# Kernel optimization log

Measured on AMD Instinct MI355X. Metric: run time of the kernel, lower is better.

## Reference

```python
import jax, jax.numpy as jnp
import numpy as np

RADIUS = 1.0
NSAMPLE = 32


def setup_inputs() -> dict:
    key = jax.random.key(0)
    k1, k2, k3, k4, k5 = jax.random.split(key, 5)
    B, Nb, M, K, C = 2, 2048, 64, 216, 32
    N = B * Nb
    # points in a 20m cube
    xyz = jax.random.uniform(k1, (N, 3), dtype=jnp.float32) * 20.0
    xyz_batch_cnt = jnp.array([Nb, Nb], dtype=jnp.int32)
    # rois: [x,y,z,dx,dy,dz,ry]
    ctr = jax.random.uniform(k2, (B, M, 3), dtype=jnp.float32) * 20.0
    dims = 1.0 + jax.random.uniform(k3, (B, M, 3), dtype=jnp.float32) * 2.0
    ry = jax.random.uniform(k4, (B, M, 1), dtype=jnp.float32) * 6.28
    rois = jnp.concatenate([ctr, dims, ry], axis=-1)
    # 6x6x6 grid points jittered around each roi center
    off = (jax.random.uniform(k5, (B, M, K, 3), dtype=jnp.float32) - 0.5) * 3.0
    new_xyz = ctr[:, :, None, :] + off
    features = jax.random.normal(jax.random.fold_in(key, 7), (N, C), dtype=jnp.float32)
    return {"xyz": xyz, "xyz_batch_cnt": xyz_batch_cnt, "new_xyz": new_xyz,
            "rois": rois, "features": features}


def _query_and_group(xyz, new_xyz, rois, features, B, Nb):
    """Ball query -> ragged compaction (padded to L=N*nsample) -> gather."""
    M, K = new_xyz.shape[1], new_xyz.shape[2]
    MK = M * K
    N = B * Nb
    L = N * NSAMPLE
    xyz_b = xyz.reshape(B, Nb, 3)
    grid = new_xyz.reshape(B, MK, 3)
    # squared distances point -> grid center, (B, Nb, MK)
    d2 = jnp.sum((xyz_b[:, :, None, :] - grid[:, None, :, :]) ** 2, axis=-1)
    # roi bounding sphere: center rois[:,:,:3], radius ||dims||_2 (the `ball` tensor)
    ctr = rois[:, :, :3]
    r2 = jnp.sum(rois[:, :, 3:6] ** 2, axis=-1)          # (B, M)
    d2b = jnp.sum((xyz_b[:, :, None, :] - ctr[:, None, :, :]) ** 2, axis=-1)  # (B,Nb,M)
    in_ball = (d2b <= r2[:, None, :])[:, :, :, None]      # (B,Nb,M,1)
    mask = (d2 <= RADIUS * RADIUS) & jnp.broadcast_to(in_ball, (B, Nb, M, K)).reshape(B, Nb, MK)
    # first-NSAMPLE-in-order selection per point (matches kernel iteration order)
    rank = jnp.cumsum(mask.astype(jnp.int32), axis=2) - 1
    cols = jnp.where(mask & (rank < NSAMPLE), rank, NSAMPLE)  # NSAMPLE = OOB -> dropped
    rows = jnp.broadcast_to(
        jnp.arange(B, dtype=jnp.int32)[:, None, None] * Nb
        + jnp.arange(Nb, dtype=jnp.int32)[None, :, None], (B, Nb, MK))
    flat_idx = jnp.broadcast_to(
        jnp.arange(B, dtype=jnp.int32)[:, None, None] * MK
        + jnp.arange(MK, dtype=jnp.int32)[None, None, :], (B, Nb, MK))
    ball_idx = jnp.full((N, NSAMPLE), -1, dtype=jnp.int32)
    ball_idx = ball_idx.at[rows.reshape(-1), cols.reshape(-1)].set(
        flat_idx.reshape(-1), mode="drop")
    # BallIndice: cumsum compaction of valid (point_idx, grid_idx) pairs, row-major
    valid = (ball_idx > -1).reshape(-1)                  # (L,)
    pos = jnp.cumsum(valid.astype(jnp.int32)) - 1
    pos_w = jnp.where(valid, pos, L)                     # invalid -> OOB -> dropped
    row_ids = jnp.broadcast_to(
        jnp.arange(N, dtype=jnp.int32)[:, None], (N, NSAMPLE)).reshape(-1)
    set_indices = jnp.zeros((L,), jnp.int32).at[pos_w].set(row_ids, mode="drop")
    set_new_indices = jnp.zeros((L,), jnp.int32).at[pos_w].set(
        ball_idx.reshape(-1), mode="drop")
    nind = jnp.sum(valid.astype(jnp.int32))
    vm = (jnp.arange(L) < nind)[:, None].astype(features.dtype)  # padding mask
    # GatherFeature (padded slots zeroed, matching new_zeros semantics)
    group_xyz = xyz[set_indices] * vm
    group_new_xyz = new_xyz.reshape(-1, 3)[set_new_indices] * vm
    group_feat = features[set_indices] * vm
    group_features = jnp.concatenate([group_xyz - group_new_xyz, group_feat], axis=1)
    return group_features, set_new_indices


def reference(xyz, xyz_batch_cnt, new_xyz, rois, features):
    B = xyz_batch_cnt.shape[0]
    Nb = xyz.shape[0] // B
    return _query_and_group(xyz, new_xyz, rois, features, B, Nb)
```

## Files before the change

kernel.cpp:

```cpp
#include <hip/hip_runtime.h>


#pragma clang fp contract(off)

typedef unsigned long long u64;

#define MAXN 4096

__global__ __launch_bounds__(256) void count_kernel(
    const float* __restrict__ xyz, const float* __restrict__ new_xyz,
    const float* __restrict__ rois, int* __restrict__ counts,
    int* __restrict__ ballidx, float* __restrict__ out_all,
    int N, int Nb, int M, int K, int nsample, int totalOut)
{
    __shared__ int plist[4][64];
    const int wave = threadIdx.x >> 6;
    const int lane = threadIdx.x & 63;
    const int r = blockIdx.x * 4 + wave;
    const u64 laneLt = (1ull << lane) - 1ull;

    {
        const int gtid = blockIdx.x * 256 + threadIdx.x;
        const int gthreads = gridDim.x * 256;
        for (int i = gtid; i < totalOut; i += gthreads) out_all[i] = 0.0f;
    }

    if (r >= N) return;

    const int b  = r / Nb;
    const float px = xyz[3 * r + 0];
    const float py = xyz[3 * r + 1];
    const float pz = xyz[3 * r + 2];

    bool pass = false;
    if (lane < M) {
        const float* rp = rois + (size_t)(b * M + lane) * 7;
        const float dx = rp[3], dy = rp[4], dz = rp[5];
        const float r2 = (dx * dx + dy * dy) + dz * dz;
        const float ex = px - rp[0], ey = py - rp[1], ez = pz - rp[2];
        pass = ((ex * ex + ey * ey) + ez * ez) <= r2;
    }
    const u64 roiMask = __ballot(pass);
    if (!roiMask) { if (lane == 0) counts[r] = 0; return; }
    if (pass) plist[wave][__popcll(roiMask & laneLt)] = lane;

    const int P = __popcll(roiMask);
    const int total = P * K;
    const float* nb_ = new_xyz + (size_t)(b * M * K) * 3;
    int* bi = ballidx + (size_t)r * nsample;

    int cnt = 0;
    for (int base = 0; base < total && cnt < nsample; base += 256) {
        bool match[4];
        int jj[4];
        #pragma unroll
        for (int u = 0; u < 4; u++) {
            const int p = base + u * 64 + lane;
            match[u] = false; jj[u] = 0;
            if (p < total) {
                const int ri = p / K;
                const int k  = p - ri * K;
                const int j  = plist[wave][ri] * K + k;
                jj[u] = j;
                const float* gp = nb_ + (size_t)j * 3;
                const float ax = px - gp[0], ay = py - gp[1], az = pz - gp[2];
                match[u] = ((ax * ax + ay * ay) + az * az) <= 1.0f;
            }
        }
        #pragma unroll
        for (int u = 0; u < 4; u++) {
            const u64 mm = __ballot(match[u]);
            const int slot = cnt + __popcll(mm & laneLt);
            if (match[u] && slot < nsample) bi[slot] = jj[u];
            cnt += __popcll(mm);
        }
    }
    if (lane == 0) counts[r] = cnt > nsample ? nsample : cnt;
}

__global__ __launch_bounds__(1024) void scan_kernel(
    const int* __restrict__ counts, int* __restrict__ offsets, int N)
{
    __shared__ int waveAux[16];
    const int t = threadIdx.x;
    const int lane = t & 63;
    const int wid = t >> 6;
    const int base = t * 4;
    int c[4];
    int s = 0;
    #pragma unroll
    for (int i = 0; i < 4; i++) {
        c[i] = (base + i < N) ? counts[base + i] : 0;
        s += c[i];
    }
    int incl = s;
    #pragma unroll
    for (int d = 1; d < 64; d <<= 1) {
        int v = __shfl_up(incl, d, 64);
        if (lane >= d) incl += v;
    }
    if (lane == 63) waveAux[wid] = incl;
    __syncthreads();
    if (t < 16) {
        int v = waveAux[t];
        #pragma unroll
        for (int d = 1; d < 16; d <<= 1) {
            int u = __shfl_up(v, d, 64);
            if (t >= d) v += u;
        }
        waveAux[t] = v;
    }
    __syncthreads();
    int run = (wid ? waveAux[wid - 1] : 0) + incl - s;
    #pragma unroll
    for (int i = 0; i < 4; i++) {
        if (base + i < N) offsets[base + i] = run;
        run += c[i];
    }
}

__global__ __launch_bounds__(256) void emit_kernel(
    const float* __restrict__ xyz, const float* __restrict__ new_xyz,
    const float* __restrict__ features,
    const int* __restrict__ counts, const int* __restrict__ offsets,
    const int* __restrict__ ballidx,
    float* __restrict__ out_feat, float* __restrict__ out_idx,
    int N, int Nb, int M, int K, int C, int nsample)
{
    const int wave = threadIdx.x >> 6;
    const int lane = threadIdx.x & 63;
    const int r = blockIdx.x * 4 + wave;
    if (r >= N) return;

    const int cnt = counts[r];
    if (cnt <= 0) return;

    const int b  = r / Nb;
    const int MK = M * K;
    const int obase = offsets[r];
    const int* bi = ballidx + (size_t)r * nsample;
    const float px = xyz[3 * r + 0];
    const float py = xyz[3 * r + 1];
    const float pz = xyz[3 * r + 2];
    const float* fr = features + (size_t)r * C;
    const float* nb_ = new_xyz + (size_t)b * MK * 3;
    const int W = 3 + C;

    float* dst = out_feat + (size_t)obase * W;
    const int tot = cnt * W;
    for (int idx = lane; idx < tot; idx += 64) {
        const int s = idx / W;
        const int c = idx - s * W;
        const int j = bi[s];
        float v;
        if (c == 0)      v = px - nb_[(size_t)j * 3 + 0];
        else if (c == 1) v = py - nb_[(size_t)j * 3 + 1];
        else if (c == 2) v = pz - nb_[(size_t)j * 3 + 2];
        else             v = fr[c - 3];
        dst[idx] = v;
    }
    for (int s = lane; s < cnt; s += 64)
        out_idx[obase + s] = (float)(b * MK + bi[s]);
}

extern "C" void kernel_launch(void* const* d_in, const int* in_sizes, int n_in,
                              void* d_out, int out_size, void* d_ws, size_t ws_size,
                              hipStream_t stream) {
    if (n_in < 5) return;

    int bc = 0;
    for (int i = 1; i < n_in; i++) if (in_sizes[i] < in_sizes[bc]) bc = i;
    const int B = in_sizes[bc];
    if (B < 1) return;

    int xi = -1, nwi = -1, ri = -1, fi = -1;
    int N = 0, M = 0, K = 0, C = 0, nsample = 0;

    for (int rr = 0; rr < n_in && xi < 0; rr++) {
        if (rr == bc) continue;
        if (in_sizes[rr] % (7 * B)) continue;
        const int M_ = in_sizes[rr] / (7 * B);
        if (M_ < 1 || M_ > 64) continue;
        for (int xx = 0; xx < n_in && xi < 0; xx++) {
            if (xx == bc || xx == rr) continue;
            if (in_sizes[xx] % 3) continue;
            const int N_ = in_sizes[xx] / 3;
            if (N_ < B || N_ % B || N_ > MAXN) continue;
            for (int nn = 0; nn < n_in && xi < 0; nn++) {
                if (nn == bc || nn == rr || nn == xx) continue;
                if (in_sizes[nn] % (3 * B * M_)) continue;
                const int K_ = in_sizes[nn] / (3 * B * M_);
                if (K_ < 1) continue;
                for (int ff = 0; ff < n_in && xi < 0; ff++) {
                    if (ff == bc || ff == rr || ff == xx || ff == nn) continue;
                    if (in_sizes[ff] % N_) continue;
                    const int C_ = in_sizes[ff] / N_;
                    if (C_ < 1) continue;
                    if (out_size % (4 + C_)) continue;
                    const long long L_ = (long long)out_size / (4 + C_);
                    if (L_ % N_) continue;
                    const int ns = (int)(L_ / N_);
                    if (ns < 1 || ns > 1024) continue;
                    xi = xx; nwi = nn; ri = rr; fi = ff;
                    N = N_; M = M_; K = K_; C = C_; nsample = ns;
                }
            }
        }
    }
    if (xi < 0) return;

    const float* xyz      = (const float*)d_in[xi];
    const float* new_xyz  = (const float*)d_in[nwi];
    const float* rois     = (const float*)d_in[ri];
    const float* features = (const float*)d_in[fi];
    const int Nb = N / B;

    const size_t L      = (size_t)N * nsample;
    const size_t chunk0 = L * (size_t)(3 + C);
    const int totalOut  = (int)(chunk0 + L);

    float* out_feat = (float*)d_out;
    float* out_idx  = out_feat + chunk0;

    const size_t wsNeed = ((size_t)2 * N + (size_t)N * nsample) * sizeof(int);
    if (ws_size < wsNeed) return;
    int* counts  = (int*)d_ws;
    int* offsets = counts + N;
    int* ballidx = offsets + N;

    const int blocks = (N + 3) / 4;

    count_kernel<<<blocks, 256, 0, stream>>>(
        xyz, new_xyz, rois, counts, ballidx, out_feat,
        N, Nb, M, K, nsample, totalOut);
    scan_kernel<<<1, 1024, 0, stream>>>(counts, offsets, N);
    emit_kernel<<<blocks, 256, 0, stream>>>(
        xyz, new_xyz, features, counts, offsets, ballidx,
        out_feat, out_idx, N, Nb, M, K, C, nsample);
}
```

Before: 90.98 us.

## Fuse prefix scan into emit kernel and vectorize output zeroing with float4

Removes the separate single-block scan kernel: every emit block now recomputes the full exclusive prefix sum of per-point counts in shared memory before writing its rows, saving one launch and a global offsets buffer. The zero-fill of the output in count_kernel now uses float4 stores instead of scalar stores, with a hipMemset fallback when the size is not a multiple of four. The cost is that all 1024 emit blocks redundantly read the 4096 counts and perform the scan, and a 16 KB shared array may lower occupancy.

```diff
diff --git a/kernel.cpp b/kernel.cpp
--- a/kernel.cpp
+++ b/kernel.cpp
@@ -10,8 +10,8 @@
 __global__ __launch_bounds__(256) void count_kernel(
     const float* __restrict__ xyz, const float* __restrict__ new_xyz,
     const float* __restrict__ rois, int* __restrict__ counts,
-    int* __restrict__ ballidx, float* __restrict__ out_all,
-    int N, int Nb, int M, int K, int nsample, int totalOut)
+    int* __restrict__ ballidx, float4* __restrict__ out_vec4,
+    int N, int Nb, int M, int K, int nsample, int totalOut4)
 {
     __shared__ int plist[4][64];
     const int wave = threadIdx.x >> 6;
@@ -22,7 +22,8 @@
     {
         const int gtid = blockIdx.x * 256 + threadIdx.x;
         const int gthreads = gridDim.x * 256;
-        for (int i = gtid; i < totalOut; i += gthreads) out_all[i] = 0.0f;
+        const float4 z = make_float4(0.f, 0.f, 0.f, 0.f);
+        for (int i = gtid; i < totalOut4; i += gthreads) out_vec4[i] = z;
     }
 
     if (r >= N) return;
@@ -78,19 +79,27 @@
     if (lane == 0) counts[r] = cnt > nsample ? nsample : cnt;
 }
 
-__global__ __launch_bounds__(1024) void scan_kernel(
-    const int* __restrict__ counts, int* __restrict__ offsets, int N)
+__global__ __launch_bounds__(256) void emit_kernel(
+    const float* __restrict__ xyz, const float* __restrict__ new_xyz,
+    const float* __restrict__ features,
+    const int* __restrict__ counts, const int* __restrict__ ballidx,
+    float* __restrict__ out_feat, float* __restrict__ out_idx,
+    int N, int Nb, int M, int K, int C, int nsample)
 {
-    __shared__ int waveAux[16];
+    __shared__ int offs[MAXN];
+    __shared__ int waveAux[4];
+
     const int t = threadIdx.x;
+    const int wave = t >> 6;
     const int lane = t & 63;
-    const int wid = t >> 6;
-    const int base = t * 4;
-    int c[4];
+
+    const int G = (N + 255) / 256;
+    const int start = t * G;
+    int c[32];
     int s = 0;
-    #pragma unroll
-    for (int i = 0; i < 4; i++) {
-        c[i] = (base + i < N) ? counts[base + i] : 0;
+    for (int i = 0; i < G; i++) {
+        const int idx = start + i;
+        c[i] = (idx < N) ? counts[idx] : 0;
         s += c[i];
     }
     int incl = s;
@@ -99,45 +108,30 @@
         int v = __shfl_up(incl, d, 64);
         if (lane >= d) incl += v;
     }
-    if (lane == 63) waveAux[wid] = incl;
+    if (lane == 63) waveAux[wave] = incl;
     __syncthreads();
-    if (t < 16) {
-        int v = waveAux[t];
+    if (t == 0) {
+        int acc = 0;
         #pragma unroll
-        for (int d = 1; d < 16; d <<= 1) {
-            int u = __shfl_up(v, d, 64);
-            if (t >= d) v += u;
-        }
-        waveAux[t] = v;
+        for (int w = 0; w < 4; w++) { int tmp = waveAux[w]; waveAux[w] = acc; acc += tmp; }
     }
     __syncthreads();
-    int run = (wid ? waveAux[wid - 1] : 0) + incl - s;
-    #pragma unroll
-    for (int i = 0; i < 4; i++) {
-        if (base + i < N) offsets[base + i] = run;
+    int run = waveAux[wave] + incl - s;
+    for (int i = 0; i < G; i++) {
+        const int idx = start + i;
+        if (idx < N) offs[idx] = run;
         run += c[i];
     }
-}
-
-__global__ __launch_bounds__(256) void emit_kernel(
-    const float* __restrict__ xyz, const float* __restrict__ new_xyz,
-    const float* __restrict__ features,
-    const int* __restrict__ counts, const int* __restrict__ offsets,
-    const int* __restrict__ ballidx,
-    float* __restrict__ out_feat, float* __restrict__ out_idx,
-    int N, int Nb, int M, int K, int C, int nsample)
-{
-    const int wave = threadIdx.x >> 6;
-    const int lane = threadIdx.x & 63;
+    __syncthreads();
+
     const int r = blockIdx.x * 4 + wave;
     if (r >= N) return;
-
     const int cnt = counts[r];
     if (cnt <= 0) return;
 
     const int b  = r / Nb;
     const int MK = M * K;
-    const int obase = offsets[r];
+    const int obase = offs[r];
     const int* bi = ballidx + (size_t)r * nsample;
     const float px = xyz[3 * r + 0];
     const float py = xyz[3 * r + 1];
@@ -149,18 +143,18 @@
     float* dst = out_feat + (size_t)obase * W;
     const int tot = cnt * W;
     for (int idx = lane; idx < tot; idx += 64) {
-        const int s = idx / W;
-        const int c = idx - s * W;
-        const int j = bi[s];
+        const int s2 = idx / W;
+        const int cc = idx - s2 * W;
+        const int j = bi[s2];
         float v;
-        if (c == 0)      v = px - nb_[(size_t)j * 3 + 0];
-        else if (c == 1) v = py - nb_[(size_t)j * 3 + 1];
-        else if (c == 2) v = pz - nb_[(size_t)j * 3 + 2];
-        else             v = fr[c - 3];
+        if (cc == 0)      v = px - nb_[(size_t)j * 3 + 0];
+        else if (cc == 1) v = py - nb_[(size_t)j * 3 + 1];
+        else if (cc == 2) v = pz - nb_[(size_t)j * 3 + 2];
+        else              v = fr[cc - 3];
         dst[idx] = v;
     }
-    for (int s = lane; s < cnt; s += 64)
-        out_idx[obase + s] = (float)(b * MK + bi[s]);
+    for (int s2 = lane; s2 < cnt; s2 += 64)
+        out_idx[obase + s2] = (float)(b * MK + bi[s2]);
 }
 
 extern "C" void kernel_launch(void* const* d_in, const int* in_sizes, int n_in,
@@ -201,6 +195,7 @@
                     if (L_ % N_) continue;
                     const int ns = (int)(L_ / N_);
                     if (ns < 1 || ns > 1024) continue;
+                    if ((N_ + 255) / 256 > 16) continue;
                     xi = xx; nwi = nn; ri = rr; fi = ff;
                     N = N_; M = M_; K = K_; C = C_; nsample = ns;
                 }
@@ -217,24 +212,29 @@
 
     const size_t L      = (size_t)N * nsample;
     const size_t chunk0 = L * (size_t)(3 + C);
-    const int totalOut  = (int)(chunk0 + L);
+    const size_t totalOut = chunk0 + L;
 
     float* out_feat = (float*)d_out;
     float* out_idx  = out_feat + chunk0;
 
-    const size_t wsNeed = ((size_t)2 * N + (size_t)N * nsample) * sizeof(int);
+    const size_t wsNeed = ((size_t)N + (size_t)N * nsample) * sizeof(int);
     if (ws_size < wsNeed) return;
     int* counts  = (int*)d_ws;
-    int* offsets = counts + N;
-    int* ballidx = offsets + N;
+    int* ballidx = counts + N;
 
     const int blocks = (N + 3) / 4;
 
-    count_kernel<<<blocks, 256, 0, stream>>>(
-        xyz, new_xyz, rois, counts, ballidx, out_feat,
-        N, Nb, M, K, nsample, totalOut);
-    scan_kernel<<<1, 1024, 0, stream>>>(counts, offsets, N);
+    if (totalOut % 4 == 0) {
+        count_kernel<<<blocks, 256, 0, stream>>>(
+            xyz, new_xyz, rois, counts, ballidx, (float4*)d_out,
+            N, Nb, M, K, nsample, (int)(totalOut / 4));
+    } else {
+        (void)hipMemsetAsync(d_out, 0, totalOut * sizeof(float), stream);
+        count_kernel<<<blocks, 256, 0, stream>>>(
+            xyz, new_xyz, rois, counts, ballidx, (float4*)d_out,
+            N, Nb, M, K, nsample, 0);
+    }
     emit_kernel<<<blocks, 256, 0, stream>>>(
-        xyz, new_xyz, features, counts, offsets, ballidx,
+        xyz, new_xyz, features, counts, ballidx,
         out_feat, out_idx, N, Nb, M, K, C, nsample);
 }
```

After: 96.70 us. 1.06x slower.
